# Performance work log

Hardware: AMD Instinct MI355X
Metric: run time of the kernel (lower is better)

The kernel has to match this reference:

```python
import jax, jax.numpy as jnp
import numpy as np

EPS = 1e-5  # BatchNorm eps (torch default)


def _norm_adj(adj):
    # DenseGCNConv: add self-loops, symmetric degree normalization
    N = adj.shape[-1]
    adj = adj + jnp.eye(N, dtype=adj.dtype)
    d = jnp.clip(adj.sum(-1), 1.0, None) ** -0.5
    return d[..., :, None] * adj * d[..., None, :]


def _gcn(x, adj_norm, W, b):
    return jnp.einsum('bij,bjf->bif', adj_norm, x @ W) + b


def _batchnorm(h, gamma, beta):
    # torch BatchNorm1d in training mode over flattened (B*N, C)
    B, N, C = h.shape
    hf = h.reshape(B * N, C)
    mu = hf.mean(0)
    var = hf.var(0)  # biased, as used for normalization
    out = (hf - mu) * jax.lax.rsqrt(var + EPS) * gamma + beta
    return out.reshape(B, N, C)


def setup_inputs() -> dict:
    key = jax.random.key(0)
    ks = jax.random.split(key, 24)
    B, N, F, H, D = 4, 256, 6, 128, 256
    s = 0.05
    a = jax.random.uniform(ks[1], (B, N, N), dtype=jnp.float32)
    adj = ((a + jnp.swapaxes(a, 1, 2)) / 2 < 0.1).astype(jnp.float32)  # sparse symmetric adjacency
    return {
        'x': jax.random.normal(ks[0], (B, N, F), dtype=jnp.float32),
        'adj': adj,
        'W1': jax.random.normal(ks[2], (F, H)) * s, 'b1': jnp.zeros((H,)),
        'W2': jax.random.normal(ks[3], (H, H)) * s, 'b2': jnp.zeros((H,)),
        'W3': jax.random.normal(ks[4], (H, D)) * s, 'b3': jnp.zeros((D,)),
        'g1': jnp.ones((H,)), 'beta1': jnp.zeros((H,)),
        'g2': jnp.ones((H,)), 'beta2': jnp.zeros((H,)),
        'e1w': jax.random.normal(ks[5], (2 * D, H)) * s, 'e1b': jnp.zeros((H,)),
        'e2w': jax.random.normal(ks[6], (H, H // 2)) * s, 'e2b': jnp.zeros((H // 2,)),
        'e3w': jax.random.normal(ks[7], (H // 2, 1)) * s, 'e3b': jnp.zeros((1,)),
        'f1w': jax.random.normal(ks[8], (D, H)) * s, 'f1b': jnp.zeros((H,)),
        'f2w': jax.random.normal(ks[9], (H, H)) * s, 'f2b': jnp.zeros((H,)),
        'f3w': jax.random.normal(ks[10], (H, F)) * s, 'f3b': jnp.zeros((F,)),
    }


def reference(x, adj, W1, b1, W2, b2, W3, b3, g1, beta1, g2, beta2,
              e1w, e1b, e2w, e2b, e3w, e3b, f1w, f1b, f2w, f2b, f3w, f3b):
    adj_norm = _norm_adj(adj)
    h = jax.nn.relu(_batchnorm(_gcn(x, adj_norm, W1, b1), g1, beta1))
    h = jax.nn.relu(_batchnorm(_gcn(h, adj_norm, W2, b2), g2, beta2))
    h = jax.nn.relu(_gcn(h, adj_norm, W3, b3))  # [B,N,D]
    D = h.shape[-1]
    # AdjacencyDecoder: Linear(cat(h_i,h_j)) == h_i@e1w[:D] + h_j@e1w[D:] (fused form, same math)
    hi = h @ e1w[:D]   # [B,N,H]
    hj = h @ e1w[D:]   # [B,N,H]
    p = jax.nn.relu(hi[:, :, None, :] + hj[:, None, :, :] + e1b)  # [B,N,N,H]
    p = jax.nn.relu(p @ e2w + e2b)                                 # [B,N,N,H/2]
    logits = (p @ e3w + e3b)[..., 0]                               # [B,N,N]
    logits = (logits + jnp.swapaxes(logits, 1, 2)) / 2
    adj_pred = jax.nn.sigmoid(logits)
    # FeatureDecoder
    f = jax.nn.relu(h @ f1w + f1b)
    f = jax.nn.relu(f @ f2w + f2b)
    feat_pred = f @ f3w + f3b
    return adj_pred, feat_pred
```

## Files before the change

kernel.cpp:

```cpp
#include <hip/hip_runtime.h>


typedef float v4f __attribute__((ext_vector_type(4)));
typedef short v8s __attribute__((ext_vector_type(8)));

__device__ __forceinline__ unsigned short f2bs(float f) {
    union { float f; unsigned int u; } v;
    v.f = f;
    return (unsigned short)((v.u + 0x7fffu + ((v.u >> 16) & 1u)) >> 16);
}

__global__ void k_pre(const float* x, const float* W1, const float* adj,
                      const float* e2w, float* buf, float* dg,
                      unsigned short* bfr_g, float* st) {
    __shared__ float ss[256];
    int blk = blockIdx.x, tid = threadIdx.x;
    if (blk < 512) {
        int idx = blk * 256 + tid;
        int m = idx >> 7, n = idx & 127;
        float s = 0.f;
        for (int k = 0; k < 6; k++) s += x[m * 6 + k] * W1[k * 128 + n];
        buf[idx] = s;
    } else if (blk < 768) {
        int row = (blk - 512) * 4 + (tid >> 6);
        int lane = tid & 63;
        const float* ap = adj + (long)row * 256;
        ss[tid] = ap[lane] + ap[lane + 64] + ap[lane + 128] + ap[lane + 192];
        __syncthreads();
        for (int o = 32; o > 0; o >>= 1) {
            if (lane < o) ss[tid] += ss[tid + o];
            __syncthreads();
        }
        if (lane == 0) {
            float t = ss[tid] + 1.f;
            if (t < 1.f) t = 1.f;
            dg[row] = rsqrtf(t);
        }
    } else {
        for (int s = tid; s < 8192; s += 256) {
            int k = s >> 6, n = s & 63;
            int kc = k >> 5, q = (k & 31) >> 3, t = k & 7;
            int nt = n >> 4, c2 = n & 15;
            bfr_g[(((nt * 4 + kc) * 64) + q * 16 + c2) * 8 + t] = f2bs(e2w[s]);
        }
        st[tid] = 0.f;
        st[256 + tid] = 0.f;
    }
}

template <int K>
__device__ __forceinline__ void dev_tile(
        int t, const float* A, const float* B, const float* bias,
        const float* dgA, float* anOut,
        const float* stat, const float* g, const float* beta,
        float* ostat, float* C,
        int N, int relu,
        int sA, int sB, int sC, int tiles_n, int tiles_m,
        float* smem) {
    constexpr int strideA = K + 4;
    constexpr int NCH = K / 16;
    float* As = smem;
    float* Bs = smem + 4160;
    int tid = threadIdx.x;
    int n2 = tid & 15, ml = tid >> 4;
    int bx = t % tiles_n;
    int tmp = t / tiles_n;
    int by = tmp % tiles_m;
    int bz = tmp / tiles_m;
    int m0 = by * 16, n0 = bx * 32;
    const float* Ab = A + (long)bz * sA;
    const float* Bb = B + (long)bz * sB;
    float* Cb = C + (long)bz * sC;
    const float* dgb = (dgA != 0) ? (dgA + bz * 256) : 0;

    int kk = tid & 15, mm = tid >> 4;
    int nb = tid & 31, kb = tid >> 5;

    float b0_r[NCH], b1_r[NCH], a_r[NCH];
    const float* Arow = Ab + (long)(m0 + mm) * K;
    #pragma unroll
    for (int i = 0; i < NCH; i++) {
        a_r[i]  = Arow[i * 16 + kk];
        b0_r[i] = Bb[(long)(i * 16 + kb) * N + n0 + nb];
        b1_r[i] = Bb[(long)(i * 16 + kb + 8) * N + n0 + nb];
    }

    if (dgA != 0) {
        float di = dgb[m0 + mm];
        float d_r[NCH];
        #pragma unroll
        for (int i = 0; i < NCH; i++) d_r[i] = dgb[i * 16 + kk];
        #pragma unroll
        for (int i = 0; i < NCH; i++) {
            int kg = i * 16 + kk;
            float v = a_r[i];
            if (m0 + mm == kg) v += 1.f;
            v = di * v * d_r[i];
            if (anOut != 0 && bx == 0)
                anOut[bz * 65536 + (m0 + mm) * 256 + kg] = v;
            As[mm * strideA + kg] = v;
        }
    } else if (stat != 0) {
        float s_r[NCH], q_r[NCH], g_r[NCH], be_r[NCH];
        #pragma unroll
        for (int i = 0; i < NCH; i++) {
            int kg = i * 16 + kk;
            s_r[i]  = stat[kg];
            q_r[i]  = stat[128 + kg];
            g_r[i]  = g[kg];
            be_r[i] = beta[kg];
        }
        #pragma unroll
        for (int i = 0; i < NCH; i++) {
            int kg = i * 16 + kk;
            float mu = s_r[i] * (1.f / 1024.f);
            float vr = q_r[i] * (1.f / 1024.f) - mu * mu;
            float sc = rsqrtf(vr + 1e-5f) * g_r[i];
            float v = (a_r[i] - mu) * sc + be_r[i];
            if (v < 0.f) v = 0.f;
            As[mm * strideA + kg] = v;
        }
    } else {
        #pragma unroll
        for (int i = 0; i < NCH; i++)
            As[mm * strideA + i * 16 + kk] = a_r[i];
    }
    #pragma unroll
    for (int i = 0; i < NCH; i++) {
        Bs[(i * 16 + kb) * 32 + nb] = b0_r[i];
        Bs[(i * 16 + kb + 8) * 32 + nb] = b1_r[i];
    }
    __syncthreads();

    float c0a = 0.f, c0b = 0.f, c1a = 0.f, c1b = 0.f;
    const float* arow = As + ml * strideA;
    const float* bcol = Bs + n2 * 2;
    #pragma unroll
    for (int q0 = 0; q0 < K; q0 += 4) {
        float4 av = *(const float4*)(arow + q0);
        float2 b0 = *(const float2*)(bcol + (q0 + 0) * 32);
        float2 b1 = *(const float2*)(bcol + (q0 + 1) * 32);
        float2 b2 = *(const float2*)(bcol + (q0 + 2) * 32);
        float2 b3 = *(const float2*)(bcol + (q0 + 3) * 32);
        c0a += av.x * b0.x; c1a += av.x * b0.y;
        c0b += av.y * b1.x; c1b += av.y * b1.y;
        c0a += av.z * b2.x; c1a += av.z * b2.y;
        c0b += av.w * b3.x; c1b += av.w * b3.y;
    }
    float c0 = c0a + c0b, c1 = c1a + c1b;
    int mRow = m0 + ml, nn = n0 + n2 * 2;
    if (bias != 0) { c0 += bias[nn]; c1 += bias[nn + 1]; }
    if (relu) {
        if (c0 < 0.f) c0 = 0.f;
        if (c1 < 0.f) c1 = 0.f;
    }
    Cb[(long)mRow * N + nn] = c0;
    Cb[(long)mRow * N + nn + 1] = c1;

    if (ostat != 0) {
        float* sred = smem;
        float* qred = smem + 544;
        __syncthreads();
        sred[(n2 * 2) * 17 + ml] = c0;
        sred[(n2 * 2 + 1) * 17 + ml] = c1;
        qred[(n2 * 2) * 17 + ml] = c0 * c0;
        qred[(n2 * 2 + 1) * 17 + ml] = c1 * c1;
        __syncthreads();
        if (tid < 32) {
            float s = 0.f, q = 0.f;
            for (int u = 0; u < 16; u++) {
                s += sred[tid * 17 + u];
                q += qred[tid * 17 + u];
            }
            atomicAdd(&ostat[n0 + tid], s);
            atomicAdd(&ostat[128 + n0 + tid], q);
        }
    }
}

template <int K>
__global__ __launch_bounds__(256, 3) void k_tgemm(
        const float* A, const float* B, const float* bias,
        const float* dgA, float* anOut,
        const float* stat, const float* g, const float* beta,
        float* ostat, float* C,
        int N, int relu,
        int sA, int sB, int sC, int tiles_n, int tiles_m) {
    __shared__ float smem[12352];
    dev_tile<K>(blockIdx.x, A, B, bias, dgA, anOut, stat, g, beta, ostat, C,
                N, relu, sA, sB, sC, tiles_n, tiles_m, smem);
}

__global__ __launch_bounds__(256, 3) void k_g67(
        const float* hb, const float* e1w, float* hi,
        const float* f1w, const float* f1b, float* f1) {
    __shared__ float smem[12352];
    int t = blockIdx.x;
    if (t < 512) {
        dev_tile<256>(t, hb, e1w, 0, 0, 0, 0, 0, 0, 0, hi,
                      128, 0, 0, 32768, 131072, 4, 64, smem);
    } else {
        dev_tile<256>(t - 512, hb, f1w, f1b, 0, 0, 0, 0, 0, 0, f1,
                      128, 1, 0, 0, 0, 4, 64, smem);
    }
}

__global__ void k_decf(const float* hi, const float* hj, const float* e1b,
                       const unsigned short* bfr_g, const float* e2b,
                       const float* e3w, const float* e3b,
                       const float* f1, const float* f2w, const float* f2b_,
                       const float* f3w, const float* f3b,
                       float* lg, float* out) {
    __shared__ float smem[4608];
    int tid = threadIdx.x;
    int blk = blockIdx.x;
    if (blk < 1024) {
        float* red = smem;
        float* pre_sh = smem + 4352;
        int lane = tid & 63, wv = tid >> 6;
        int col = lane & 15, quad = lane >> 4;
        int bi = blk, b = bi >> 8;
        if (tid < 128) pre_sh[tid] = hi[bi * 128 + tid] + e1b[tid];
        __syncthreads();
        float e2bv[4], e3wv[4];
        for (int nt = 0; nt < 4; nt++) {
            e2bv[nt] = e2b[nt * 16 + col];
            e3wv[nt] = e3w[nt * 16 + col];
        }
        const float* hjb = hj + b * 32768;
        #pragma unroll 1
        for (int ms = 0; ms < 4; ms++) {
            v4f acc[4];
            for (int nt = 0; nt < 4; nt++) {
                v4f z = {0.f, 0.f, 0.f, 0.f};
                acc[nt] = z;
            }
            int j = wv * 64 + ms * 16 + col;
            const float* rowp = hjb + j * 128 + quad * 8;
            #pragma unroll 1
            for (int kc = 0; kc < 4; kc++) {
                const float* pp = pre_sh + kc * 32 + quad * 8;
                const float* hp = rowp + kc * 32;
                v8s af;
                #pragma unroll
                for (int t = 0; t < 8; t++) {
                    float p = pp[t] + hp[t];
                    p = (p > 0.f) ? p : 0.f;
                    af[t] = (short)f2bs(p);
                }
                #pragma unroll
                for (int nt = 0; nt < 4; nt++) {
                    v8s bf = *(const v8s*)&bfr_g[(((nt * 4 + kc) * 64) + lane) * 8];
                    acc[nt] = __builtin_amdgcn_mfma_f32_16x16x32_bf16(
                        af, bf, acc[nt], 0, 0, 0);
                }
            }
            #pragma unroll
            for (int r = 0; r < 4; r++) {
                float s = 0.f;
                #pragma unroll
                for (int nt = 0; nt < 4; nt++) {
                    float v = acc[nt][r] + e2bv[nt];
                    if (v > 0.f) s += v * e3wv[nt];
                }
                red[(wv * 64 + ms * 16 + quad * 4 + r) * 17 + col] = s;
            }
        }
        __syncthreads();
        float s = e3b[0];
        for (int c = 0; c < 16; c++) s += red[tid * 17 + c];
        lg[bi * 256 + tid] = s;
    } else {
        float* f2row = smem;
        int r0 = (blk - 1024) * 4;
        for (int p = 0; p < 2; p++) {
            int idx = tid + p * 256;
            int r = r0 + (idx >> 7), n = idx & 127;
            const float* f1r = f1 + (long)r * 128;
            float s0 = 0.f, s1 = 0.f, s2 = 0.f, s3 = 0.f;
            #pragma unroll
            for (int k = 0; k < 128; k += 4) {
                float4 fv = *(const float4*)(f1r + k);
                s0 += fv.x * f2w[(k + 0) * 128 + n];
                s1 += fv.y * f2w[(k + 1) * 128 + n];
                s2 += fv.z * f2w[(k + 2) * 128 + n];
                s3 += fv.w * f2w[(k + 3) * 128 + n];
            }
            float s = f2b_[n] + ((s0 + s1) + (s2 + s3));
            if (s < 0.f) s = 0.f;
            f2row[idx] = s;
        }
        __syncthreads();
        if (tid < 24) {
            int r = tid / 6, c = tid % 6;
            float s = f3b[c];
            const float* fr = f2row + r * 128;
            for (int k = 0; k < 128; k++) s += fr[k] * f3w[k * 6 + c];
            out[262144 + (r0 + r) * 6 + c] = s;
        }
    }
}

__global__ void k_symsig(const float* lg, float* out) {
    __shared__ float Ta[32 * 33];
    __shared__ float Tb[32 * 33];
    int tid = threadIdx.x;
    int b = blockIdx.x / 36;
    int t = blockIdx.x % 36;
    int ti = 0, rem = t;
    while (rem >= 8 - ti) { rem -= 8 - ti; ti++; }
    int tj = ti + rem;
    int i0 = ti * 32, j0 = tj * 32;
    const float* lgb = lg + b * 65536;
    for (int p = 0; p < 4; p++) {
        int idx = p * 256 + tid;
        int r = idx >> 5, c = idx & 31;
        Ta[r * 33 + c] = lgb[(i0 + r) * 256 + j0 + c];
        Tb[r * 33 + c] = lgb[(j0 + r) * 256 + i0 + c];
    }
    __syncthreads();
    float* ob = out + b * 65536;
    for (int p = 0; p < 4; p++) {
        int idx = p * 256 + tid;
        int r = idx >> 5, c = idx & 31;
        float v1 = 0.5f * (Ta[r * 33 + c] + Tb[c * 33 + r]);
        ob[(i0 + r) * 256 + j0 + c] = 1.f / (1.f + expf(-v1));
        float v2 = 0.5f * (Tb[r * 33 + c] + Ta[c * 33 + r]);
        ob[(j0 + r) * 256 + i0 + c] = 1.f / (1.f + expf(-v2));
    }
}

extern "C" void kernel_launch(void* const* d_in, const int* in_sizes, int n_in,
                              void* d_out, int out_size, void* d_ws, size_t ws_size,
                              hipStream_t stream) {
    const float* x   = (const float*)d_in[0];
    const float* adj = (const float*)d_in[1];
    const float* W1  = (const float*)d_in[2];
    const float* b1  = (const float*)d_in[3];
    const float* W2  = (const float*)d_in[4];
    const float* b2  = (const float*)d_in[5];
    const float* W3  = (const float*)d_in[6];
    const float* b3  = (const float*)d_in[7];
    const float* g1  = (const float*)d_in[8];
    const float* be1 = (const float*)d_in[9];
    const float* g2  = (const float*)d_in[10];
    const float* be2 = (const float*)d_in[11];
    const float* e1w = (const float*)d_in[12];
    const float* e1b = (const float*)d_in[13];
    const float* e2w = (const float*)d_in[14];
    const float* e2b = (const float*)d_in[15];
    const float* e3w = (const float*)d_in[16];
    const float* e3b = (const float*)d_in[17];
    const float* f1w = (const float*)d_in[18];
    const float* f1b = (const float*)d_in[19];
    const float* f2w = (const float*)d_in[20];
    const float* f2b_ = (const float*)d_in[21];
    const float* f3w = (const float*)d_in[22];
    const float* f3b = (const float*)d_in[23];

    float* out = (float*)d_out;

    if (ws_size < (size_t)1600000 * 4) {
        hipMemsetAsync(d_out, 0x60, 4096, stream);
        return;
    }
    float* ws = (float*)d_ws;
    float* st1 = ws;
    float* st2 = ws + 256;
    float* dg  = ws + 512;
    unsigned short* bfr_g = (unsigned short*)(ws + 1536);
    float* An  = ws + 5632;
    float* buf = An + 262144;
    float* hb  = buf + 262144;
    float* lg  = hb + 262144;
    float* h1  = lg + 262144;
    float* h2  = h1 + 131072;
    float* hi  = h2 + 131072;
    float* hj  = hi + 131072;

    k_pre<<<769, 256, 0, stream>>>(x, W1, adj, e2w, buf, dg, bfr_g, st1);
    k_tgemm<256><<<256, 256, 0, stream>>>(adj, buf, b1, dg, An, 0, 0, 0, st1, h1,
                                          128, 0, 65536, 32768, 32768, 4, 16);
    k_tgemm<128><<<256, 256, 0, stream>>>(h1, W2, 0, 0, 0, st1, g1, be1, 0, buf,
                                          128, 0, 0, 0, 0, 4, 64);
    k_tgemm<256><<<256, 256, 0, stream>>>(An, buf, b2, 0, 0, 0, 0, 0, st2, h2,
                                          128, 0, 65536, 32768, 32768, 4, 16);
    k_tgemm<128><<<512, 256, 0, stream>>>(h2, W3, 0, 0, 0, st2, g2, be2, 0, buf,
                                          256, 0, 0, 0, 0, 8, 64);
    k_tgemm<256><<<512, 256, 0, stream>>>(An, buf, b3, 0, 0, 0, 0, 0, 0, hb,
                                          256, 1, 65536, 65536, 65536, 8, 16);
    k_g67<<<768, 256, 0, stream>>>(hb, e1w, hi, f1w, f1b, h1);
    k_decf<<<1280, 256, 0, stream>>>(hi, hj, e1b, bfr_g, e2b, e3w, e3b,
                                     h1, f2w, f2b_, f3w, f3b, lg, out);
    k_symsig<<<144, 256, 0, stream>>>(lg, out);
}
```

Before: 187.2 us.

## Fuse all stages into one persistent cooperative kernel with grid syncs

Wraps each stage body in a device function and runs the whole pipeline in a single cooperative kernel of 512 blocks, separated by grid-wide syncs, with the old multi-launch path kept as a fallback if the cooperative launch fails. The aim is to remove per-kernel launch and drain gaps between nine launches. In exchange, phases with fewer tiles leave blocks idle, occupancy is capped at two blocks per CU, and each grid sync adds its own barrier cost.

```diff
diff --git a/kernel.cpp b/kernel.cpp
--- a/kernel.cpp
+++ b/kernel.cpp
@@ -1,4 +1,7 @@
 #include <hip/hip_runtime.h>
+#include <hip/hip_cooperative_groups.h>
+
+namespace cg = cooperative_groups;
 
 
 typedef float v4f __attribute__((ext_vector_type(4)));
@@ -10,11 +13,9 @@
     return (unsigned short)((v.u + 0x7fffu + ((v.u >> 16) & 1u)) >> 16);
 }
 
-__global__ void k_pre(const float* x, const float* W1, const float* adj,
-                      const float* e2w, float* buf, float* dg,
-                      unsigned short* bfr_g, float* st) {
-    __shared__ float ss[256];
-    int blk = blockIdx.x, tid = threadIdx.x;
+__device__ __forceinline__ void pre_unit(int blk, int tid,
+        const float* x, const float* W1, const float* adj, const float* e2w,
+        float* buf, float* dg, unsigned short* bfr_g, float* st, float* ss) {
     if (blk < 512) {
         int idx = blk * 256 + tid;
         int m = idx >> 7, n = idx & 127;
@@ -178,42 +179,14 @@
     }
 }
 
-template <int K>
-__global__ __launch_bounds__(256, 3) void k_tgemm(
-        const float* A, const float* B, const float* bias,
-        const float* dgA, float* anOut,
-        const float* stat, const float* g, const float* beta,
-        float* ostat, float* C,
-        int N, int relu,
-        int sA, int sB, int sC, int tiles_n, int tiles_m) {
-    __shared__ float smem[12352];
-    dev_tile<K>(blockIdx.x, A, B, bias, dgA, anOut, stat, g, beta, ostat, C,
-                N, relu, sA, sB, sC, tiles_n, tiles_m, smem);
-}
-
-__global__ __launch_bounds__(256, 3) void k_g67(
-        const float* hb, const float* e1w, float* hi,
-        const float* f1w, const float* f1b, float* f1) {
-    __shared__ float smem[12352];
-    int t = blockIdx.x;
-    if (t < 512) {
-        dev_tile<256>(t, hb, e1w, 0, 0, 0, 0, 0, 0, 0, hi,
-                      128, 0, 0, 32768, 131072, 4, 64, smem);
-    } else {
-        dev_tile<256>(t - 512, hb, f1w, f1b, 0, 0, 0, 0, 0, 0, f1,
-                      128, 1, 0, 0, 0, 4, 64, smem);
-    }
-}
-
-__global__ void k_decf(const float* hi, const float* hj, const float* e1b,
-                       const unsigned short* bfr_g, const float* e2b,
-                       const float* e3w, const float* e3b,
-                       const float* f1, const float* f2w, const float* f2b_,
-                       const float* f3w, const float* f3b,
-                       float* lg, float* out) {
-    __shared__ float smem[4608];
+__device__ __forceinline__ void dec_unit(int blk,
+        const float* hi, const float* hj, const float* e1b,
+        const unsigned short* bfr_g, const float* e2b,
+        const float* e3w, const float* e3b,
+        const float* f1, const float* f2w, const float* f2b_,
+        const float* f3w, const float* f3b,
+        float* lg, float* out, float* smem) {
     int tid = threadIdx.x;
-    int blk = blockIdx.x;
     if (blk < 1024) {
         float* red = smem;
         float* pre_sh = smem + 4352;
@@ -301,12 +274,13 @@
     }
 }
 
-__global__ void k_symsig(const float* lg, float* out) {
-    __shared__ float Ta[32 * 33];
-    __shared__ float Tb[32 * 33];
+__device__ __forceinline__ void symsig_unit(int blk, const float* lg,
+                                            float* out, float* smem) {
+    float* Ta = smem;
+    float* Tb = smem + 32 * 33;
     int tid = threadIdx.x;
-    int b = blockIdx.x / 36;
-    int t = blockIdx.x % 36;
+    int b = blk / 36;
+    int t = blk % 36;
     int ti = 0, rem = t;
     while (rem >= 8 - ti) { rem -= 8 - ti; ti++; }
     int tj = ti + rem;
@@ -328,6 +302,114 @@
         float v2 = 0.5f * (Tb[r * 33 + c] + Ta[c * 33 + r]);
         ob[(j0 + r) * 256 + i0 + c] = 1.f / (1.f + expf(-v2));
     }
+}
+
+struct P {
+    const float *x, *adj, *W1, *b1, *W2, *b2, *W3, *b3, *g1, *be1, *g2, *be2;
+    const float *e1w, *e1b, *e2w, *e2b, *e3w, *e3b;
+    const float *f1w, *f1b, *f2w, *f2b, *f3w, *f3b;
+    float* out;
+    float *st1, *st2, *dg;
+    unsigned short* bfr_g;
+    float *An, *buf, *hb, *lg, *h1, *h2, *hi, *hj;
+};
+
+__global__ __launch_bounds__(256, 2) void k_fused(P p) {
+    __shared__ float smem[12352];
+    cg::grid_group grid = cg::this_grid();
+    int bid = blockIdx.x, tid = threadIdx.x;
+
+    for (int u = bid; u < 769; u += 512) {
+        pre_unit(u, tid, p.x, p.W1, p.adj, p.e2w, p.buf, p.dg, p.bfr_g, p.st1, smem);
+        __syncthreads();
+    }
+    grid.sync();
+    if (bid < 256)
+        dev_tile<256>(bid, p.adj, p.buf, p.b1, p.dg, p.An, 0, 0, 0, p.st1, p.h1,
+                      128, 0, 65536, 32768, 32768, 4, 16, smem);
+    grid.sync();
+    if (bid < 256)
+        dev_tile<128>(bid, p.h1, p.W2, 0, 0, 0, p.st1, p.g1, p.be1, 0, p.buf,
+                      128, 0, 0, 0, 0, 4, 64, smem);
+    grid.sync();
+    if (bid < 256)
+        dev_tile<256>(bid, p.An, p.buf, p.b2, 0, 0, 0, 0, 0, p.st2, p.h2,
+                      128, 0, 65536, 32768, 32768, 4, 16, smem);
+    grid.sync();
+    dev_tile<128>(bid, p.h2, p.W3, 0, 0, 0, p.st2, p.g2, p.be2, 0, p.buf,
+                  256, 0, 0, 0, 0, 8, 64, smem);
+    grid.sync();
+    dev_tile<256>(bid, p.An, p.buf, p.b3, 0, 0, 0, 0, 0, 0, p.hb,
+                  256, 1, 65536, 65536, 65536, 8, 16, smem);
+    grid.sync();
+    for (int u = bid; u < 768; u += 512) {
+        if (u < 512)
+            dev_tile<256>(u, p.hb, p.e1w, 0, 0, 0, 0, 0, 0, 0, p.hi,
+                          128, 0, 0, 32768, 131072, 4, 64, smem);
+        else
+            dev_tile<256>(u - 512, p.hb, p.f1w, p.f1b, 0, 0, 0, 0, 0, 0, p.h1,
+                          128, 1, 0, 0, 0, 4, 64, smem);
+        __syncthreads();
+    }
+    grid.sync();
+    for (int u = bid; u < 1280; u += 512) {
+        dec_unit(u, p.hi, p.hj, p.e1b, p.bfr_g, p.e2b, p.e3w, p.e3b,
+                 p.h1, p.f2w, p.f2b, p.f3w, p.f3b, p.lg, p.out, smem);
+        __syncthreads();
+    }
+    grid.sync();
+    if (bid < 144)
+        symsig_unit(bid, p.lg, p.out, smem);
+}
+
+__global__ void k_pre(const float* x, const float* W1, const float* adj,
+                      const float* e2w, float* buf, float* dg,
+                      unsigned short* bfr_g, float* st) {
+    __shared__ float ss[256];
+    pre_unit(blockIdx.x, threadIdx.x, x, W1, adj, e2w, buf, dg, bfr_g, st, ss);
+}
+
+template <int K>
+__global__ __launch_bounds__(256, 3) void k_tgemm(
+        const float* A, const float* B, const float* bias,
+        const float* dgA, float* anOut,
+        const float* stat, const float* g, const float* beta,
+        float* ostat, float* C,
+        int N, int relu,
+        int sA, int sB, int sC, int tiles_n, int tiles_m) {
+    __shared__ float smem[12352];
+    dev_tile<K>(blockIdx.x, A, B, bias, dgA, anOut, stat, g, beta, ostat, C,
+                N, relu, sA, sB, sC, tiles_n, tiles_m, smem);
+}
+
+__global__ __launch_bounds__(256, 3) void k_g67(
+        const float* hb, const float* e1w, float* hi,
+        const float* f1w, const float* f1b, float* f1) {
+    __shared__ float smem[12352];
+    int t = blockIdx.x;
+    if (t < 512) {
+        dev_tile<256>(t, hb, e1w, 0, 0, 0, 0, 0, 0, 0, hi,
+                      128, 0, 0, 32768, 131072, 4, 64, smem);
+    } else {
+        dev_tile<256>(t - 512, hb, f1w, f1b, 0, 0, 0, 0, 0, 0, f1,
+                      128, 1, 0, 0, 0, 4, 64, smem);
+    }
+}
+
+__global__ void k_decf(const float* hi, const float* hj, const float* e1b,
+                       const unsigned short* bfr_g, const float* e2b,
+                       const float* e3w, const float* e3b,
+                       const float* f1, const float* f2w, const float* f2b_,
+                       const float* f3w, const float* f3b,
+                       float* lg, float* out) {
+    __shared__ float smem[4608];
+    dec_unit(blockIdx.x, hi, hj, e1b, bfr_g, e2b, e3w, e3b,
+             f1, f2w, f2b_, f3w, f3b, lg, out, smem);
+}
+
+__global__ void k_symsig(const float* lg, float* out) {
+    __shared__ float smem[2 * 32 * 33];
+    symsig_unit(blockIdx.x, lg, out, smem);
 }
 
 extern "C" void kernel_launch(void* const* d_in, const int* in_sizes, int n_in,
@@ -378,6 +460,23 @@
     float* hi  = h2 + 131072;
     float* hj  = hi + 131072;
 
+    P prm;
+    prm.x = x; prm.adj = adj; prm.W1 = W1; prm.b1 = b1; prm.W2 = W2; prm.b2 = b2;
+    prm.W3 = W3; prm.b3 = b3; prm.g1 = g1; prm.be1 = be1; prm.g2 = g2; prm.be2 = be2;
+    prm.e1w = e1w; prm.e1b = e1b; prm.e2w = e2w; prm.e2b = e2b; prm.e3w = e3w; prm.e3b = e3b;
+    prm.f1w = f1w; prm.f1b = f1b; prm.f2w = f2w; prm.f2b = f2b_; prm.f3w = f3w; prm.f3b = f3b;
+    prm.out = out;
+    prm.st1 = st1; prm.st2 = st2; prm.dg = dg; prm.bfr_g = bfr_g;
+    prm.An = An; prm.buf = buf; prm.hb = hb; prm.lg = lg;
+    prm.h1 = h1; prm.h2 = h2; prm.hi = hi; prm.hj = hj;
+
+    void* args[] = { (void*)&prm };
+    hipError_t err = hipLaunchCooperativeKernel((const void*)k_fused,
+                                                dim3(512), dim3(256),
+                                                args, 0, stream);
+    if (err == hipSuccess) return;
+    (void)hipGetLastError();
+
     k_pre<<<769, 256, 0, stream>>>(x, W1, adj, e2w, buf, dg, bfr_g, st1);
     k_tgemm<256><<<256, 256, 0, stream>>>(adj, buf, b1, dg, An, 0, 0, 0, st1, h1,
                                           128, 0, 65536, 32768, 32768, 4, 16);
```

New measurement: 648.6 us. 246% more time.

## Fuse GCN layers 2-3 and decoder projections into two reassociated mid kernels

Applied to the files above, without the earlier changes.

Replaces five launches (two tgemm feature transforms, two adjacency GEMMs and the hi/hj/f1 projection kernel) with two k_mid launches. Each block applies BN+ReLU while staging its input, computes An@(BN(h)) first and then multiplies by W. This reassociation avoids writing intermediate buffers to global memory. The layer-3 variant also computes hi, hj and f1 in-block from the output held in shared memory. The tradeoff is only 64 blocks of 512 threads using scalar FP32 FMAs with W read straight from global memory, so the GPU is much less occupied and the path has less throughput than the tiled GEMMs.

```diff
diff --git a/kernel.cpp b/kernel.cpp
--- a/kernel.cpp
+++ b/kernel.cpp
@@ -191,17 +191,173 @@
                 N, relu, sA, sB, sC, tiles_n, tiles_m, smem);
 }
 
-__global__ __launch_bounds__(256, 3) void k_g67(
-        const float* hb, const float* e1w, float* hi,
-        const float* f1w, const float* f1b, float* f1) {
-    __shared__ float smem[12352];
-    int t = blockIdx.x;
-    if (t < 512) {
-        dev_tile<256>(t, hb, e1w, 0, 0, 0, 0, 0, 0, 0, hi,
-                      128, 0, 0, 32768, 131072, 4, 64, smem);
-    } else {
-        dev_tile<256>(t - 512, hb, f1w, f1b, 0, 0, 0, 0, 0, 0, f1,
-                      128, 1, 0, 0, 0, 4, 64, smem);
+template <int NW, int STATS, int RELU, int G67>
+__global__ __launch_bounds__(512, 1) void k_mid(
+        const float* __restrict__ An, const float* __restrict__ Hin,
+        const float* __restrict__ W, const float* __restrict__ bias,
+        const float* __restrict__ st, const float* __restrict__ g,
+        const float* __restrict__ beta, float* ostat, float* OUT,
+        const float* __restrict__ e1w, const float* __restrict__ f1w,
+        const float* __restrict__ f1b,
+        float* hi, float* hj, float* f1) {
+    __shared__ float sm[10752];
+    float* sl  = sm;
+    float* sh  = sm + 128;
+    float* An_s = sm + 256;
+    float* P_s  = sm + 4416;
+    float* T_s  = sm + 8640;
+
+    int t = threadIdx.x;
+    int bz = blockIdx.x >> 4, mt = blockIdx.x & 15;
+    int m0 = mt * 16;
+    int r = t >> 5, cg = t & 31;
+
+    if (t < 128) {
+        float mu = st[t] * (1.f / 1024.f);
+        float vr = st[128 + t] * (1.f / 1024.f) - mu * mu;
+        float sc = rsqrtf(vr + 1e-5f) * g[t];
+        sl[t] = sc;
+        sh[t] = beta[t] - mu * sc;
+    }
+    {
+        const float* Ag = An + (long)bz * 65536 + (long)m0 * 256 + t * 8;
+        float4 a0 = *(const float4*)Ag;
+        float4 a1 = *(const float4*)(Ag + 4);
+        float* d = An_s + r * 260 + cg * 8;
+        d[0] = a0.x; d[1] = a0.y; d[2] = a0.z; d[3] = a0.w;
+        d[4] = a1.x; d[5] = a1.y; d[6] = a1.z; d[7] = a1.w;
+    }
+
+    float4 acc = {0.f, 0.f, 0.f, 0.f};
+    for (int p = 0; p < 8; ++p) {
+        __syncthreads();
+        {
+            int kl = t >> 4, c = (t & 15) * 8;
+            const float* src = Hin + (long)bz * 32768 + (p * 32 + kl) * 128 + c;
+            float4 v0 = *(const float4*)src;
+            float4 v1 = *(const float4*)(src + 4);
+            float* d = P_s + kl * 132 + c;
+            float o;
+            o = v0.x * sl[c + 0] + sh[c + 0]; d[0] = o > 0.f ? o : 0.f;
+            o = v0.y * sl[c + 1] + sh[c + 1]; d[1] = o > 0.f ? o : 0.f;
+            o = v0.z * sl[c + 2] + sh[c + 2]; d[2] = o > 0.f ? o : 0.f;
+            o = v0.w * sl[c + 3] + sh[c + 3]; d[3] = o > 0.f ? o : 0.f;
+            o = v1.x * sl[c + 4] + sh[c + 4]; d[4] = o > 0.f ? o : 0.f;
+            o = v1.y * sl[c + 5] + sh[c + 5]; d[5] = o > 0.f ? o : 0.f;
+            o = v1.z * sl[c + 6] + sh[c + 6]; d[6] = o > 0.f ? o : 0.f;
+            o = v1.w * sl[c + 7] + sh[c + 7]; d[7] = o > 0.f ? o : 0.f;
+        }
+        __syncthreads();
+        const float* ar = An_s + r * 260 + p * 32;
+        #pragma unroll
+        for (int kk = 0; kk < 32; ++kk) {
+            float a = ar[kk];
+            float4 pv = *(const float4*)(P_s + kk * 132 + cg * 4);
+            acc.x += a * pv.x; acc.y += a * pv.y;
+            acc.z += a * pv.z; acc.w += a * pv.w;
+        }
+    }
+    {
+        float* d = T_s + r * 132 + cg * 4;
+        d[0] = acc.x; d[1] = acc.y; d[2] = acc.z; d[3] = acc.w;
+    }
+    __syncthreads();
+
+    float4 o0 = *(const float4*)(bias + cg * 4);
+    float4 o1 = {0.f, 0.f, 0.f, 0.f};
+    if (NW == 256) o1 = *(const float4*)(bias + 128 + cg * 4);
+    const float* tr = T_s + r * 132;
+    #pragma unroll 4
+    for (int c = 0; c < 128; ++c) {
+        float tv = tr[c];
+        const float4 w0 = *(const float4*)(W + (long)c * NW + cg * 4);
+        o0.x += tv * w0.x; o0.y += tv * w0.y;
+        o0.z += tv * w0.z; o0.w += tv * w0.w;
+        if (NW == 256) {
+            const float4 w1 = *(const float4*)(W + (long)c * NW + 128 + cg * 4);
+            o1.x += tv * w1.x; o1.y += tv * w1.y;
+            o1.z += tv * w1.z; o1.w += tv * w1.w;
+        }
+    }
+
+    if (STATS) {
+        float* red_s = An_s;
+        float* red_q = P_s;
+        red_s[(cg * 4 + 0) * 17 + r] = o0.x;
+        red_s[(cg * 4 + 1) * 17 + r] = o0.y;
+        red_s[(cg * 4 + 2) * 17 + r] = o0.z;
+        red_s[(cg * 4 + 3) * 17 + r] = o0.w;
+        red_q[(cg * 4 + 0) * 17 + r] = o0.x * o0.x;
+        red_q[(cg * 4 + 1) * 17 + r] = o0.y * o0.y;
+        red_q[(cg * 4 + 2) * 17 + r] = o0.z * o0.z;
+        red_q[(cg * 4 + 3) * 17 + r] = o0.w * o0.w;
+        __syncthreads();
+        if (t < 128) {
+            float s = 0.f, q = 0.f;
+            #pragma unroll
+            for (int u = 0; u < 16; ++u) {
+                s += red_s[t * 17 + u];
+                q += red_q[t * 17 + u];
+            }
+            atomicAdd(&ostat[t], s);
+            atomicAdd(&ostat[128 + t], q);
+        }
+    }
+
+    if (RELU) {
+        if (o0.x < 0.f) o0.x = 0.f;
+        if (o0.y < 0.f) o0.y = 0.f;
+        if (o0.z < 0.f) o0.z = 0.f;
+        if (o0.w < 0.f) o0.w = 0.f;
+        if (NW == 256) {
+            if (o1.x < 0.f) o1.x = 0.f;
+            if (o1.y < 0.f) o1.y = 0.f;
+            if (o1.z < 0.f) o1.z = 0.f;
+            if (o1.w < 0.f) o1.w = 0.f;
+        }
+    }
+
+    if (OUT != 0) {
+        if (NW == 128) {
+            float* d = OUT + (long)bz * 32768 + (long)(m0 + r) * 128 + cg * 4;
+            *(float4*)d = o0;
+        } else {
+            float* d = OUT + (long)bz * 65536 + (long)(m0 + r) * 256 + cg * 4;
+            *(float4*)d = o0;
+            *(float4*)(d + 128) = o1;
+        }
+    }
+
+    if (G67) {
+        float* hb_s = An_s;
+        float* d = hb_s + r * 260 + cg * 4;
+        d[0] = o0.x; d[1] = o0.y; d[2] = o0.z; d[3] = o0.w;
+        d[128] = o1.x; d[129] = o1.y; d[130] = o1.z; d[131] = o1.w;
+        __syncthreads();
+        const float* hr = hb_s + r * 260;
+        #pragma unroll 1
+        for (int pass = 0; pass < 3; ++pass) {
+            const float* Wc = (pass == 0) ? e1w
+                            : (pass == 1) ? (e1w + 32768) : f1w;
+            float4 a = {0.f, 0.f, 0.f, 0.f};
+            if (pass == 2) a = *(const float4*)(f1b + cg * 4);
+            #pragma unroll 4
+            for (int c = 0; c < 256; ++c) {
+                float hv = hr[c];
+                const float4 w4 = *(const float4*)(Wc + (long)c * 128 + cg * 4);
+                a.x += hv * w4.x; a.y += hv * w4.y;
+                a.z += hv * w4.z; a.w += hv * w4.w;
+            }
+            if (pass == 2) {
+                if (a.x < 0.f) a.x = 0.f;
+                if (a.y < 0.f) a.y = 0.f;
+                if (a.z < 0.f) a.z = 0.f;
+                if (a.w < 0.f) a.w = 0.f;
+            }
+            float* dst = ((pass == 0) ? hi : (pass == 1) ? hj : f1)
+                         + ((long)bz * 256 + m0 + r) * 128 + cg * 4;
+            *(float4*)dst = a;
+        }
     }
 }
 
@@ -381,15 +537,10 @@
     k_pre<<<769, 256, 0, stream>>>(x, W1, adj, e2w, buf, dg, bfr_g, st1);
     k_tgemm<256><<<256, 256, 0, stream>>>(adj, buf, b1, dg, An, 0, 0, 0, st1, h1,
                                           128, 0, 65536, 32768, 32768, 4, 16);
-    k_tgemm<128><<<256, 256, 0, stream>>>(h1, W2, 0, 0, 0, st1, g1, be1, 0, buf,
-                                          128, 0, 0, 0, 0, 4, 64);
-    k_tgemm<256><<<256, 256, 0, stream>>>(An, buf, b2, 0, 0, 0, 0, 0, st2, h2,
-                                          128, 0, 65536, 32768, 32768, 4, 16);
-    k_tgemm<128><<<512, 256, 0, stream>>>(h2, W3, 0, 0, 0, st2, g2, be2, 0, buf,
-                                          256, 0, 0, 0, 0, 8, 64);
-    k_tgemm<256><<<512, 256, 0, stream>>>(An, buf, b3, 0, 0, 0, 0, 0, 0, hb,
-                                          256, 1, 65536, 65536, 65536, 8, 16);
-    k_g67<<<768, 256, 0, stream>>>(hb, e1w, hi, f1w, f1b, h1);
+    k_mid<128, 1, 0, 0><<<64, 512, 0, stream>>>(
+        An, h1, W2, b2, st1, g1, be1, st2, h2, 0, 0, 0, 0, 0, 0);
+    k_mid<256, 0, 1, 1><<<64, 512, 0, stream>>>(
+        An, h2, W3, b3, st2, g2, be2, 0, 0, e1w, f1w, f1b, hi, hj, h1);
     k_decf<<<1280, 256, 0, stream>>>(hi, hj, e1b, bfr_g, e2b, e3w, e3b,
                                      h1, f2w, f2b_, f3w, f3b, lg, out);
     k_symsig<<<144, 256, 0, stream>>>(lg, out);
```

New measurement: 253.5 us. 35.4% more time.
